# Kernel optimization log

Measured on AMD Instinct MI355X. Metric: run time of the kernel, lower is better.

Reference implementation:

```python
import jax, jax.numpy as jnp
import numpy as np

BATCH = 2048
NUM_FIELDS = 32
EMBED = 64
NPAIRS = NUM_FIELDS * (NUM_FIELDS - 1) // 2  # 496
# static pair indices (i < j), same order as the torch double loop
ROW, COL = np.triu_indices(NUM_FIELDS, k=1)
ROW = jnp.asarray(ROW)
COL = jnp.asarray(COL)


def setup_inputs() -> dict:
    key = jax.random.key(0)
    k1, k2 = jax.random.split(key)
    emb_inputs = jax.random.normal(k1, (BATCH, NUM_FIELDS, EMBED), dtype=jnp.float32)
    # xavier_normal_ on kernel of shape (E, NC2, E): fan_in = NC2*E (dims[1:]), fan_out = E*E... 
    # torch: fan_in = size(1)*receptive = NPAIRS*EMBED? torch uses size(1)*prod(size[2:]) = NPAIRS*EMBED,
    # fan_out = size(0)*prod(size[2:]) = EMBED*EMBED; std = sqrt(2/(fan_in+fan_out))
    fan_in = NPAIRS * EMBED
    fan_out = EMBED * EMBED
    std = float(np.sqrt(2.0 / (fan_in + fan_out)))
    kernel = jax.random.normal(k2, (EMBED, NPAIRS, EMBED), dtype=jnp.float32) * std
    return {"emb_inputs": emb_inputs, "kernel": kernel}


def reference(emb_inputs, kernel):
    # emb_inputs: (B, N, E); kernel: (E, NC2, E)
    p = emb_inputs[:, ROW]  # (B, NC2, E)
    q = emb_inputs[:, COL]  # (B, NC2, E)
    # torch: kp[b,i,pair] = sum_j p[b,pair,j] * kernel[i,pair,j]; out[b,pair] = sum_i kp*q
    kp = jnp.einsum('bpj,ipj->bpi', p, kernel)  # (B, NC2, E) -- avoids (B,E,NC2,E) blowup
    outputs = jnp.sum(kp * q, axis=-1)          # (B, NC2)
    return outputs[:, None, :]                  # (B, 1, NC2)
```

## Files before the change

### kernel.cpp

```cpp
#include <hip/hip_runtime.h>
#include <hip/hip_bf16.h>

#define BATCH   2048
#define NFIELDS 32
#define EMBED   64
#define NPAIRS  496
#define BT      512
#define NIT     8
#define TPB     32

typedef __attribute__((ext_vector_type(8))) short bf16x8;
typedef __attribute__((ext_vector_type(4))) float f32x4;

__device__ __forceinline__ unsigned short f2bf(float x) {
    unsigned int u = __float_as_uint(x);
    unsigned int r = 0x7fffu + ((u >> 16) & 1u);
    return (unsigned short)((u + r) >> 16);
}

#define PP_OFF 0
#define PQ_OFF 4194304
#define KB_OFF 8388608
#define WS_ELEMS 10420224

__global__ __launch_bounds__(256) void prepass(
    const float* __restrict__ emb, const float* __restrict__ kern,
    unsigned short* __restrict__ ws)
{
    unsigned short* pp = ws + PP_OFF;
    unsigned short* pq = ws + PQ_OFF;
    unsigned short* kb = ws + KB_OFF;
    const int NEMB8 = BATCH * NFIELDS * EMBED / 8;
    const int NKER8 = EMBED * NPAIRS * EMBED / 8;
    int v = blockIdx.x * blockDim.x + threadIdx.x;
    if (v < NEMB8) {
        int base = v * 8;
        int e0 = base & 63;
        int f  = (base >> 6) & 31;
        int b  = base >> 11;
        float4 v0 = *(const float4*)(emb + base);
        float4 v1 = *(const float4*)(emb + base + 4);
        ushort4 lo, hi;
        lo.x = f2bf(v0.x); lo.y = f2bf(v0.y); lo.z = f2bf(v0.z); lo.w = f2bf(v0.w);
        hi.x = f2bf(v1.x); hi.y = f2bf(v1.y); hi.z = f2bf(v1.z); hi.w = f2bf(v1.w);
        int t = b >> 4, col = b & 15;
        int ks = e0 >> 5, quad = (e0 & 31) >> 3;
        size_t dp = (size_t)f * 131072 + t * 1024 + ks * 512 + quad * 128 + col * 8;
        *(ushort4*)(pp + dp)     = lo;
        *(ushort4*)(pp + dp + 4) = hi;
        int pos  = e0 & 31;
        int half = pos >> 4;
        int qq   = (pos & 15) >> 2;
        size_t dq = (size_t)f * 131072 + t * 1024 + ks * 512 + qq * 128 + col * 8 + half * 4;
        *(ushort4*)(pq + dq)       = lo;
        *(ushort4*)(pq + dq + 128) = hi;
    } else if (v < NEMB8 + NKER8) {
        int base = (v - NEMB8) * 8;
        int j0 = base & 63;
        int pr = (base >> 6) % NPAIRS;
        int i  = (base >> 6) / NPAIRS;
        float4 v0 = *(const float4*)(kern + base);
        float4 v1 = *(const float4*)(kern + base + 4);
        ushort4 lo, hi;
        lo.x = f2bf(v0.x); lo.y = f2bf(v0.y); lo.z = f2bf(v0.z); lo.w = f2bf(v0.w);
        hi.x = f2bf(v1.x); hi.y = f2bf(v1.y); hi.z = f2bf(v1.z); hi.w = f2bf(v1.w);
        size_t dk = (size_t)pr * 4096 + i * 64 + j0;
        *(ushort4*)(kb + dk)     = lo;
        *(ushort4*)(kb + dk + 4) = hi;
    }
}

__global__ __launch_bounds__(256) void opn_main(
    const unsigned short* __restrict__ ws, float* __restrict__ out)
{
    const unsigned short* pp = ws + PP_OFF;
    const unsigned short* pq = ws + PQ_OFF;
    const unsigned short* kb = ws + KB_OFF;

    const int pair = blockIdx.x;
    const int bt   = blockIdx.y;
    int r = 0, s0 = 0;
    while (pair >= s0 + (NFIELDS - 1 - r)) { s0 += NFIELDS - 1 - r; ++r; }
    const int c = r + 1 + (pair - s0);

    const int tid = threadIdx.x;
    const int wave = tid >> 6, lane = tid & 63;
    const int col = lane & 15, quad = lane >> 4;

    bf16x8 kfr[4][2];
    const unsigned short* kp = kb + (size_t)pair * 4096;
    #pragma unroll
    for (int mt = 0; mt < 4; ++mt)
        #pragma unroll
        for (int ks = 0; ks < 2; ++ks)
            kfr[mt][ks] = *(const bf16x8*)(kp + (mt*16 + col)*64 + ks*32 + quad*8);

    const int T0 = bt * TPB + wave * NIT;
    const unsigned short* pbase = pp + (size_t)r * 131072 + (size_t)T0 * 1024 + lane * 8;
    const unsigned short* qbase = pq + (size_t)c * 131072 + (size_t)T0 * 1024 + lane * 8;

    bf16x8 pA[2], pB[2];
    uint4  qA[2], qB[2];
    pA[0] = *(const bf16x8*)(pbase);
    pB[0] = *(const bf16x8*)(pbase + 512);
    qA[0] = *(const uint4*)(qbase);
    qB[0] = *(const uint4*)(qbase + 512);

    #pragma unroll
    for (int it = 0; it < NIT; ++it) {
        const int cur = it & 1, nxt = cur ^ 1;
        if (it + 1 < NIT) {
            pA[nxt] = *(const bf16x8*)(pbase + (it+1)*1024);
            pB[nxt] = *(const bf16x8*)(pbase + (it+1)*1024 + 512);
            qA[nxt] = *(const uint4*)(qbase + (it+1)*1024);
            qB[nxt] = *(const uint4*)(qbase + (it+1)*1024 + 512);
        }

        f32x4 acc[4];
        #pragma unroll
        for (int mt = 0; mt < 4; ++mt) {
            acc[mt] = (f32x4){0.f, 0.f, 0.f, 0.f};
            acc[mt] = __builtin_amdgcn_mfma_f32_16x16x32_bf16(kfr[mt][0], pA[cur], acc[mt], 0, 0, 0);
            acc[mt] = __builtin_amdgcn_mfma_f32_16x16x32_bf16(kfr[mt][1], pB[cur], acc[mt], 0, 0, 0);
        }

        float partial = 0.f;
        {
            uint4 qa = qA[cur], qb = qB[cur];
            partial += acc[0][0] * __uint_as_float(qa.x << 16);
            partial += acc[0][1] * __uint_as_float(qa.x & 0xffff0000u);
            partial += acc[0][2] * __uint_as_float(qa.y << 16);
            partial += acc[0][3] * __uint_as_float(qa.y & 0xffff0000u);
            partial += acc[1][0] * __uint_as_float(qa.z << 16);
            partial += acc[1][1] * __uint_as_float(qa.z & 0xffff0000u);
            partial += acc[1][2] * __uint_as_float(qa.w << 16);
            partial += acc[1][3] * __uint_as_float(qa.w & 0xffff0000u);
            partial += acc[2][0] * __uint_as_float(qb.x << 16);
            partial += acc[2][1] * __uint_as_float(qb.x & 0xffff0000u);
            partial += acc[2][2] * __uint_as_float(qb.y << 16);
            partial += acc[2][3] * __uint_as_float(qb.y & 0xffff0000u);
            partial += acc[3][0] * __uint_as_float(qb.z << 16);
            partial += acc[3][1] * __uint_as_float(qb.z & 0xffff0000u);
            partial += acc[3][2] * __uint_as_float(qb.w << 16);
            partial += acc[3][3] * __uint_as_float(qb.w & 0xffff0000u);
        }
        partial += __shfl_xor(partial, 16, 64);
        partial += __shfl_xor(partial, 32, 64);

        if (quad == 0)
            out[(size_t)((T0 + it) * 16 + col) * NPAIRS + pair] = partial;
    }
}

__global__ __launch_bounds__(256) void opn_naive(
    const float* __restrict__ emb, const float* __restrict__ kern,
    float* __restrict__ out)
{
    int idx = blockIdx.x * blockDim.x + threadIdx.x;
    if (idx >= BATCH * NPAIRS) return;
    int b = idx / NPAIRS, p = idx % NPAIRS;
    int r = 0, s0 = 0;
    while (p >= s0 + (NFIELDS - 1 - r)) { s0 += NFIELDS - 1 - r; ++r; }
    int c = r + 1 + (p - s0);
    const float* pv = emb + ((size_t)b * NFIELDS + r) * EMBED;
    const float* qv = emb + ((size_t)b * NFIELDS + c) * EMBED;
    float acc = 0.f;
    for (int i = 0; i < EMBED; ++i) {
        const float* kr = kern + ((size_t)i * NPAIRS + p) * EMBED;
        float kpv = 0.f;
        for (int j = 0; j < EMBED; ++j) kpv += kr[j] * pv[j];
        acc += kpv * qv[i];
    }
    out[(size_t)b * NPAIRS + p] = acc;
}

extern "C" void kernel_launch(void* const* d_in, const int* in_sizes, int n_in,
                              void* d_out, int out_size, void* d_ws, size_t ws_size,
                              hipStream_t stream) {
    const float* emb  = (const float*)d_in[0];
    const float* kern = (const float*)d_in[1];
    float* out = (float*)d_out;

    if (ws_size >= (size_t)WS_ELEMS * sizeof(unsigned short)) {
        unsigned short* ws = (unsigned short*)d_ws;
        const int NEMB8 = BATCH * NFIELDS * EMBED / 8;
        const int NKER8 = EMBED * NPAIRS * EMBED / 8;
        int total = NEMB8 + NKER8;
        prepass<<<(total + 255) / 256, 256, 0, stream>>>(emb, kern, ws);
        dim3 grid(NPAIRS, BATCH / BT);
        opn_main<<<grid, 256, 0, stream>>>(ws, out);
    } else {
        int total = BATCH * NPAIRS;
        opn_naive<<<(total + 255) / 256, 256, 0, stream>>>(emb, kern, out);
    }
}
```

Measured before the change: 111.7 us.

## Halve batch tile, remap blocks to pair groups per XCD, preload all loads

Batch tile shrinks from 512 to 256, so each block runs 4 iterations instead of 8 and the grid doubles to about 3968 blocks. The launch becomes a 1D grid whose block index is remapped so that the 8 XCD-interleaved block positions each take a contiguous range of 62 pairs, aiming for better L2 reuse of embedding rows and kernel slices within an XCD. All p/q loads are issued up front instead of double-buffered, which raises memory-level parallelism but uses more registers. Each block now reloads its kernel fragment for half as much batch work.

```diff
diff --git a/kernel.cpp b/kernel.cpp
--- a/kernel.cpp
+++ b/kernel.cpp
@@ -5,9 +5,11 @@
 #define NFIELDS 32
 #define EMBED   64
 #define NPAIRS  496
-#define BT      512
-#define NIT     8
-#define TPB     32
+#define BT      256
+#define NIT     4
+#define TPB     16
+#define NBT     (BATCH / BT)
+#define PPX     62
 
 typedef __attribute__((ext_vector_type(8))) short bf16x8;
 typedef __attribute__((ext_vector_type(4))) float f32x4;
@@ -77,8 +79,11 @@
     const unsigned short* pq = ws + PQ_OFF;
     const unsigned short* kb = ws + KB_OFF;
 
-    const int pair = blockIdx.x;
-    const int bt   = blockIdx.y;
+    const int bx   = blockIdx.x;
+    const int slot = bx >> 3;
+    const int pair = (bx & 7) * PPX + slot % PPX;
+    const int bt   = slot / PPX;
+
     int r = 0, s0 = 0;
     while (pair >= s0 + (NFIELDS - 1 - r)) { s0 += NFIELDS - 1 - r; ++r; }
     const int c = r + 1 + (pair - s0);
@@ -99,34 +104,29 @@
     const unsigned short* pbase = pp + (size_t)r * 131072 + (size_t)T0 * 1024 + lane * 8;
     const unsigned short* qbase = pq + (size_t)c * 131072 + (size_t)T0 * 1024 + lane * 8;
 
-    bf16x8 pA[2], pB[2];
-    uint4  qA[2], qB[2];
-    pA[0] = *(const bf16x8*)(pbase);
-    pB[0] = *(const bf16x8*)(pbase + 512);
-    qA[0] = *(const uint4*)(qbase);
-    qB[0] = *(const uint4*)(qbase + 512);
+    bf16x8 pA[NIT], pB[NIT];
+    uint4  qA[NIT], qB[NIT];
+    #pragma unroll
+    for (int it = 0; it < NIT; ++it) {
+        pA[it] = *(const bf16x8*)(pbase + it*1024);
+        pB[it] = *(const bf16x8*)(pbase + it*1024 + 512);
+        qA[it] = *(const uint4*)(qbase + it*1024);
+        qB[it] = *(const uint4*)(qbase + it*1024 + 512);
+    }
 
     #pragma unroll
     for (int it = 0; it < NIT; ++it) {
-        const int cur = it & 1, nxt = cur ^ 1;
-        if (it + 1 < NIT) {
-            pA[nxt] = *(const bf16x8*)(pbase + (it+1)*1024);
-            pB[nxt] = *(const bf16x8*)(pbase + (it+1)*1024 + 512);
-            qA[nxt] = *(const uint4*)(qbase + (it+1)*1024);
-            qB[nxt] = *(const uint4*)(qbase + (it+1)*1024 + 512);
-        }
-
         f32x4 acc[4];
         #pragma unroll
         for (int mt = 0; mt < 4; ++mt) {
             acc[mt] = (f32x4){0.f, 0.f, 0.f, 0.f};
-            acc[mt] = __builtin_amdgcn_mfma_f32_16x16x32_bf16(kfr[mt][0], pA[cur], acc[mt], 0, 0, 0);
-            acc[mt] = __builtin_amdgcn_mfma_f32_16x16x32_bf16(kfr[mt][1], pB[cur], acc[mt], 0, 0, 0);
+            acc[mt] = __builtin_amdgcn_mfma_f32_16x16x32_bf16(kfr[mt][0], pA[it], acc[mt], 0, 0, 0);
+            acc[mt] = __builtin_amdgcn_mfma_f32_16x16x32_bf16(kfr[mt][1], pB[it], acc[mt], 0, 0, 0);
         }
 
         float partial = 0.f;
         {
-            uint4 qa = qA[cur], qb = qB[cur];
+            uint4 qa = qA[it], qb = qB[it];
             partial += acc[0][0] * __uint_as_float(qa.x << 16);
             partial += acc[0][1] * __uint_as_float(qa.x & 0xffff0000u);
             partial += acc[0][2] * __uint_as_float(qa.y << 16);
@@ -187,8 +187,7 @@
         const int NKER8 = EMBED * NPAIRS * EMBED / 8;
         int total = NEMB8 + NKER8;
         prepass<<<(total + 255) / 256, 256, 0, stream>>>(emb, kern, ws);
-        dim3 grid(NPAIRS, BATCH / BT);
-        opn_main<<<grid, 256, 0, stream>>>(ws, out);
+        opn_main<<<dim3(NPAIRS * NBT), 256, 0, stream>>>(ws, out);
     } else {
         int total = BATCH * NPAIRS;
         opn_naive<<<(total + 255) / 256, 256, 0, stream>>>(emb, kern, out);
```

Measured after the change: 109.9 us. Within noise of the previous version (-1.7%).
